# Optimization experiments

Measured on AMD Instinct MI355X. Metric: run time of the kernel, lower is better.

## Reference

```python
import jax, jax.numpy as jnp
import numpy as np

B, T, D_IN, D_SAE, K = 256, 8, 768, 8192, 32


def setup_inputs() -> dict:
    key = jax.random.key(0)
    k1, k2, k3 = jax.random.split(key, 3)
    x = jax.random.normal(k1, (B, T, D_IN), dtype=jnp.float32)
    # kaiming_uniform: bound = sqrt(6 / fan_in), fan_in = prod of trailing dims
    bound_e = float(np.sqrt(6.0 / (D_SAE * D_IN)))
    W_enc = jax.random.uniform(k2, (T, D_SAE, D_IN), jnp.float32, -bound_e, bound_e)
    bound_d = float(np.sqrt(6.0 / (D_IN * D_SAE)))
    W_dec = jax.random.uniform(k3, (T, D_IN, D_SAE), jnp.float32, -bound_d, bound_d)
    # decoder column normalization (norm over d_in axis), as in _normalize_decoder
    norms = jnp.clip(jnp.linalg.norm(W_dec, axis=1, keepdims=True), 1e-8)
    W_dec = W_dec / norms
    b_enc = jnp.zeros((T, D_SAE), jnp.float32)
    b_dec = jnp.zeros((T, D_IN), jnp.float32)
    return {"x": x, "W_enc": W_enc, "b_enc": b_enc, "W_dec": W_dec,
            "b_dec": b_dec, "k": K}


def reference(x, W_enc, b_enc, W_dec, b_dec, k):
    # x: (B, T, d_in)
    x_c = x - b_dec[None]                                   # (B, T, d)
    pre = jnp.einsum('btd,thd->bth', x_c, W_enc) + b_enc[None]  # (B, T, h)
    bt = pre.shape[0] * pre.shape[1]
    pre_flat = pre.reshape(bt, -1)
    topk_vals, topk_idx = jax.lax.top_k(pre_flat, k)        # (BT, k)
    rows = jnp.arange(bt)[:, None]
    u_flat = jnp.zeros_like(pre_flat).at[rows, topk_idx].set(jax.nn.relu(topk_vals))
    u = u_flat.reshape(pre.shape)                            # (B, T, h)
    x_hat = jnp.einsum('bth,tdh->btd', u, W_dec) + b_dec[None]
    recon_loss = jnp.mean(jnp.sum((x_hat - x) ** 2, axis=-1))
    return recon_loss, x_hat, u
```

## Files before the change

kernel.cpp:

```cpp
#include <hip/hip_runtime.h>
#include <cstdint>
#include <cstddef>

constexpr int B_SZ  = 256;
constexpr int T_SZ  = 8;
constexpr int DIN   = 768;
constexpr int DSAE  = 8192;
constexpr int KSEL  = 32;
constexpr int NROWS = B_SZ * T_SZ;
constexpr int CAND_CAP = 64;
constexpr int RCAP  = 32;
constexpr float EPS_W = 2e-4f;

constexpr size_t XC_SZ    = (size_t)NROWS * DIN;
constexpr size_t OFF_XC   = 0;
constexpr size_t OFF_SIDX = OFF_XC + XC_SZ;
constexpr size_t OFF_SVAL = OFF_SIDX + (size_t)NROWS * KSEL;
constexpr size_t OFF_WT   = OFF_SVAL + (size_t)NROWS * KSEL;
constexpr size_t WT_WORDS = (size_t)T_SZ * DSAE * DIN / 2;
constexpr size_t WS_FAST_WORDS = OFF_WT + WT_WORDS;

typedef short bf16x8 __attribute__((ext_vector_type(8)));
typedef float f32x4  __attribute__((ext_vector_type(4)));

__device__ inline unsigned rne1(float x) {
  unsigned u = __float_as_uint(x);
  return (u + 0x7FFFu + ((u >> 16) & 1u)) >> 16;
}
__device__ inline float fromb(unsigned h) { return __uint_as_float(h << 16); }
__device__ inline float bf16tof(unsigned short v) {
  return __uint_as_float((unsigned)v << 16);
}

__global__ void k_zero(float* p) { *p = 0.f; }

__global__ __launch_bounds__(256) void k_xc(const float* __restrict__ x,
                                            const float* __restrict__ bdec,
                                            float* __restrict__ xc) {
  int n = NROWS * DIN;
  for (int i = blockIdx.x * 256 + threadIdx.x; i < n; i += gridDim.x * 256) {
    int d = i % DIN;
    int t = (i / DIN) & (T_SZ - 1);
    xc[i] = x[i] - bdec[t * DIN + d];
  }
}

__global__ __launch_bounds__(512, 2) void k_encoder_split(const float* __restrict__ xc,
                                                          const float* __restrict__ Wenc,
                                                          const float* __restrict__ benc,
                                                          float* __restrict__ pre) {
  const int t  = blockIdx.y;
  const int n0 = blockIdx.x * 256;
  constexpr int NS = DIN / 32;
  constexpr int LO = 256 * 32;
  __shared__ __align__(16) short As[2][256 * 32];
  __shared__ __align__(16) short Bs[2][256 * 32 * 2];
  const int tid = threadIdx.x;

  const int srow = tid >> 1;
  const int kh   = (tid & 1) * 16;
  const float* aG = xc   + ((size_t)srow * T_SZ + t) * DIN + kh;
  const float* bG = Wenc + ((size_t)t * DSAE + n0 + srow) * DIN + kh;
  const int ssw = (srow & 3) ^ ((srow >> 2) & 3);
  const int c0 = (kh >> 3) + 0, c1 = (kh >> 3) + 1;
  const int wOff0 = srow * 32 + ((c0 ^ ssw) << 3);
  const int wOff1 = srow * 32 + ((c1 ^ ssw) << 3);

  auto loadG = [&](const float* base, int s, float4 (&R)[4]) {
    const float* p = base + s * 32;
    R[0] = *(const float4*)p;       R[1] = *(const float4*)(p + 4);
    R[2] = *(const float4*)(p + 8); R[3] = *(const float4*)(p + 12);
  };
  auto stageA = [&](float4 (&R)[4], int buf) {
    uint4 U;
    U.x = rne1(R[0].x) | (rne1(R[0].y) << 16); U.y = rne1(R[0].z) | (rne1(R[0].w) << 16);
    U.z = rne1(R[1].x) | (rne1(R[1].y) << 16); U.w = rne1(R[1].z) | (rne1(R[1].w) << 16);
    *(uint4*)&As[buf][wOff0] = U;
    U.x = rne1(R[2].x) | (rne1(R[2].y) << 16); U.y = rne1(R[2].z) | (rne1(R[2].w) << 16);
    U.z = rne1(R[3].x) | (rne1(R[3].y) << 16); U.w = rne1(R[3].z) | (rne1(R[3].w) << 16);
    *(uint4*)&As[buf][wOff1] = U;
  };
  auto stageB = [&](float4 (&R)[4], int buf) {
    float wv[16];
    *(float4*)&wv[0] = R[0]; *(float4*)&wv[4]  = R[1];
    *(float4*)&wv[8] = R[2]; *(float4*)&wv[12] = R[3];
    unsigned hh[16], ll[16];
#pragma unroll
    for (int i = 0; i < 16; ++i) {
      unsigned h = rne1(wv[i]);
      float res = wv[i] - fromb(h);
      hh[i] = h; ll[i] = rne1(res);
    }
    uint4 U;
    U.x = hh[0] | (hh[1] << 16);  U.y = hh[2] | (hh[3] << 16);
    U.z = hh[4] | (hh[5] << 16);  U.w = hh[6] | (hh[7] << 16);
    *(uint4*)&Bs[buf][wOff0] = U;
    U.x = hh[8] | (hh[9] << 16);  U.y = hh[10] | (hh[11] << 16);
    U.z = hh[12] | (hh[13] << 16); U.w = hh[14] | (hh[15] << 16);
    *(uint4*)&Bs[buf][wOff1] = U;
    U.x = ll[0] | (ll[1] << 16);  U.y = ll[2] | (ll[3] << 16);
    U.z = ll[4] | (ll[5] << 16);  U.w = ll[6] | (ll[7] << 16);
    *(uint4*)&Bs[buf][wOff0 + LO] = U;
    U.x = ll[8] | (ll[9] << 16);  U.y = ll[10] | (ll[11] << 16);
    U.z = ll[12] | (ll[13] << 16); U.w = ll[14] | (ll[15] << 16);
    *(uint4*)&Bs[buf][wOff1 + LO] = U;
  };

  const int wid = tid >> 6, lane = tid & 63;
  const int wm = wid >> 1;
  const int wn = wid & 1;
  const int l15 = lane & 15, kc = lane >> 4;
  int aOff[4], bOff[8];
#pragma unroll
  for (int i = 0; i < 4; ++i) {
    int ra = wm * 64 + i * 16 + l15;
    aOff[i] = ra * 32 + ((kc ^ ((ra & 3) ^ ((ra >> 2) & 3))) << 3);
  }
#pragma unroll
  for (int j = 0; j < 8; ++j) {
    int rb = wn * 128 + j * 16 + l15;
    bOff[j] = rb * 32 + ((kc ^ ((rb & 3) ^ ((rb >> 2) & 3))) << 3);
  }

  f32x4 acc[4][8] = {};
  auto compute = [&](int buf) {
    __syncthreads();
#pragma unroll
    for (int pass = 0; pass < 2; ++pass) {
      const int po = pass * LO;
#pragma unroll
      for (int nh = 0; nh < 2; ++nh) {
        bf16x8 bfr[4];
#pragma unroll
        for (int q = 0; q < 4; ++q)
          bfr[q] = *(const bf16x8*)&Bs[buf][bOff[nh * 4 + q] + po];
#pragma unroll
        for (int mi = 0; mi < 4; ++mi) {
          bf16x8 a = *(const bf16x8*)&As[buf][aOff[mi]];
#pragma unroll
          for (int q = 0; q < 4; ++q)
            acc[mi][nh * 4 + q] = __builtin_amdgcn_mfma_f32_16x16x32_bf16(
                a, bfr[q], acc[mi][nh * 4 + q], 0, 0, 0);
        }
      }
    }
  };

  float4 aR[4], bR0[4], bR1[4];
  loadG(bG, 0, bR0); loadG(aG, 0, aR);
  stageA(aR, 0); stageB(bR0, 0);
  loadG(bG, 1, bR0); loadG(aG, 1, aR);
  loadG(bG, 2, bR1);
  int cur = 0;
  auto iter = [&](int s, float4 (&bR)[4]) {
    compute(cur);
    if (s + 1 < NS) {
      stageA(aR, cur ^ 1);
      stageB(bR, cur ^ 1);
      if (s + 3 < NS) loadG(bG, s + 3, bR);
      if (s + 2 < NS) loadG(aG, s + 2, aR);
    }
    cur ^= 1;
  };
  for (int s = 0; s < NS; s += 2) { iter(s, bR0); iter(s + 1, bR1); }

#pragma unroll
  for (int ni = 0; ni < 8; ++ni) {
    const int col = n0 + wn * 128 + ni * 16 + l15;
    const float bias = benc[(size_t)t * DSAE + col];
#pragma unroll
    for (int mi = 0; mi < 4; ++mi) {
      const int rbase = wm * 64 + mi * 16 + kc * 4;
#pragma unroll
      for (int j = 0; j < 4; ++j)
        pre[((size_t)(rbase + j) * T_SZ + t) * DSAE + col] = acc[mi][ni][j] + bias;
    }
  }
}

__global__ __launch_bounds__(256) void k_select(const float* __restrict__ xc,
                                                const float* __restrict__ Wenc,
                                                const float* __restrict__ benc,
                                                float* u,
                                                int* __restrict__ sel_idx,
                                                float* __restrict__ sel_val) {
  const int r = blockIdx.x, t = r & (T_SZ - 1);
  __shared__ float sp[DSAE];
  __shared__ float redf[4], redf2[4];
  __shared__ int   redi[4];
  __shared__ float cv[CAND_CAP]; __shared__ int ci[CAND_CAP];
  __shared__ float sv[CAND_CAP]; __shared__ int si[CAND_CAP];
  __shared__ float rv[RCAP];     __shared__ int ri[RCAP];
  __shared__ double rd[RCAP];
  __shared__ double xd[DIN];
  __shared__ int   s_n, s_nR, s_A, s_nW;
  const int tid = threadIdx.x, lane = tid & 63, w = tid >> 6;
  float* urow = u + (size_t)r * DSAE;

  float s1 = 0.f, s2 = 0.f;
  for (int sgm = 0; sgm < DSAE / 256; ++sgm) {
    float v = urow[tid + sgm * 256];
    sp[tid + sgm * 256] = v;
    s1 += v; s2 = fmaf(v, v, s2);
  }
  for (int off = 32; off; off >>= 1) {
    s1 += __shfl_down(s1, off); s2 += __shfl_down(s2, off);
  }
  if (lane == 0) { redf[w] = s1; redf2[w] = s2; }
  __syncthreads();
  const float mean = (redf[0] + redf[1] + redf[2] + redf[3]) * (1.f / DSAE);
  const float var  = (redf2[0] + redf2[1] + redf2[2] + redf2[3]) * (1.f / DSAE) - mean * mean;
  const float sd   = sqrtf(fmaxf(var, 1e-20f));

  auto countGE = [&](float th) -> int {
    int c = 0;
#pragma unroll
    for (int sgm = 0; sgm < DSAE / 256; ++sgm)
      c += (sp[tid + sgm * 256] >= th) ? 1 : 0;
    for (int off = 32; off; off >>= 1) c += __shfl_down(c, off);
    __syncthreads();
    if (lane == 0) redi[w] = c;
    __syncthreads();
    return redi[0] + redi[1] + redi[2] + redi[3];
  };

  float tlo = mean + 2.0f * sd, thi = mean + 3.5f * sd;
  for (int it = 0; it < 8 && countGE(tlo) < KSEL; ++it) tlo -= sd;
  float th = mean + 2.52f * sd;
  int c = countGE(th);
  for (int it = 0; it < 24 && (c < KSEL || c > CAND_CAP); ++it) {
    if (c > CAND_CAP) tlo = th; else thi = th;
    th = 0.5f * (tlo + thi);
    c = countGE(th);
  }
  if (c < KSEL) { th = tlo; c = countGE(th); }

  if (tid == 0) s_n = 0;
  __syncthreads();
  for (int sgm = 0; sgm < DSAE / 256; ++sgm) {
    int i = tid + sgm * 256;
    float v = sp[i];
    if (v >= th) {
      int p = atomicAdd(&s_n, 1);
      if (p < CAND_CAP) { cv[p] = v; ci[p] = i; }
    }
  }
  __syncthreads();
  const int n = s_n < CAND_CAP ? s_n : CAND_CAP;

  if (tid < n) {
    float v = cv[tid]; int id = ci[tid];
    int rk = 0;
    for (int j = 0; j < n; ++j) {
      float vj = cv[j];
      rk += (vj > v || (vj == v && ci[j] < id)) ? 1 : 0;
    }
    sv[rk] = v; si[rk] = id;
  }
  __syncthreads();

  const float v32 = sv[KSEL - 1];
  const float wlo = v32 - EPS_W, whi = v32 + EPS_W;
  if (tid == 0) {
    int A = 0;
    while (A < KSEL - 1 && sv[A] > whi) ++A;
    s_A = A;
    int e = A;
    while (e < n && sv[e] >= wlo) ++e;
    s_nW = e - A;
  }
  __syncthreads();
  const int A  = s_A;
  const int nW = s_nW < RCAP ? s_nW : RCAP;
  if (tid < nW) { rv[tid] = sv[A + tid]; ri[tid] = si[A + tid]; }
  if (tid == 0) s_nR = nW;
  __syncthreads();
  if (th > wlo) {
    for (int sgm = 0; sgm < DSAE / 256; ++sgm) {
      int i = tid + sgm * 256;
      float v = sp[i];
      if (v >= wlo && v < th) {
        int p = atomicAdd(&s_nR, 1);
        if (p < RCAP) { rv[p] = v; ri[p] = i; }
      }
    }
  }
  __syncthreads();
  const int nR = s_nR < RCAP ? s_nR : RCAP;

  if (nR >= 2) {
    for (int i = tid; i < DIN; i += 256) xd[i] = (double)xc[(size_t)r * DIN + i];
    __syncthreads();
    for (int j = w; j < nR; j += 4) {
      const int h = ri[j];
      const float* wrow = Wenc + ((size_t)t * DSAE + h) * DIN;
      double s = 0.0;
#pragma unroll
      for (int ss = 0; ss < DIN / 64; ++ss)
        s += xd[lane + 64 * ss] * (double)wrow[lane + 64 * ss];
      for (int off = 32; off; off >>= 1) s += __shfl_down(s, off);
      if (lane == 0) rd[j] = s + (double)benc[(size_t)t * DSAE + h];
    }
  } else if (nR == 1) {
    if (tid == 0) rd[0] = (double)rv[0];
  }
  __syncthreads();

  for (int sgm = 0; sgm < DSAE / 256; ++sgm) urow[tid + sgm * 256] = 0.f;
  __syncthreads();

  if (tid < A) {
    float val = fmaxf(sv[tid], 0.f);
    urow[si[tid]] = val;
    sel_idx[(size_t)r * KSEL + tid] = si[tid];
    sel_val[(size_t)r * KSEL + tid] = val;
  }
  const int need = KSEL - A;
  if (tid < nR) {
    double v = rd[tid]; int id = ri[tid];
    int rk = 0;
    for (int j = 0; j < nR; ++j) {
      double vj = rd[j];
      rk += (vj > v || (vj == v && ri[j] < id)) ? 1 : 0;
    }
    if (rk < need) {
      float val = fmaxf((float)v, 0.f);
      urow[id] = val;
      sel_idx[(size_t)r * KSEL + A + rk] = id;
      sel_val[(size_t)r * KSEL + A + rk] = val;
    }
  }
}

__global__ __launch_bounds__(256) void k_transpose(const float* __restrict__ W,
                                                   unsigned short* __restrict__ Wt) {
  __shared__ float s[32][33];
  const int t  = blockIdx.z;
  const int h0 = blockIdx.x * 32;
  const int d0 = blockIdx.y * 32;
  const int c  = threadIdx.x & 31, rr = threadIdx.x >> 5;
#pragma unroll
  for (int q = 0; q < 4; ++q) {
    int d = d0 + rr + q * 8;
    s[rr + q * 8][c] = W[((size_t)t * DIN + d) * DSAE + h0 + c];
  }
  __syncthreads();
#pragma unroll
  for (int q = 0; q < 4; ++q) {
    int h = h0 + rr + q * 8;
    Wt[((size_t)t * DSAE + h) * DIN + d0 + c] = (unsigned short)rne1(s[c][rr + q * 8]);
  }
}

template <bool TRANSPOSED>
__global__ __launch_bounds__(256) void k_decoder(const void* __restrict__ Wd_,
                                                 const float* __restrict__ x,
                                                 const float* __restrict__ bdec,
                                                 const int* __restrict__ sel_idx,
                                                 const float* __restrict__ sel_val,
                                                 float* __restrict__ xhat,
                                                 float* __restrict__ loss) {
  const int r = blockIdx.x, t = r & (T_SZ - 1);
  __shared__ int   si[KSEL];
  __shared__ float sv[KSEL];
  __shared__ float rbuf[4];
  const int tid = threadIdx.x;
  if (tid < KSEL) {
    si[tid] = sel_idx[(size_t)r * KSEL + tid] & (DSAE - 1);
    sv[tid] = sel_val[(size_t)r * KSEL + tid];
  }
  __syncthreads();

  float acc[3];
#pragma unroll
  for (int i = 0; i < 3; ++i) acc[i] = bdec[(size_t)t * DIN + tid + 256 * i];
#pragma unroll 4
  for (int j = 0; j < KSEL; ++j) {
    const int h = si[j];
    const float v = sv[j];
    if (TRANSPOSED) {
      const unsigned short* wrow =
          (const unsigned short*)Wd_ + ((size_t)t * DSAE + h) * DIN;
#pragma unroll
      for (int i = 0; i < 3; ++i)
        acc[i] = fmaf(v, bf16tof(wrow[tid + 256 * i]), acc[i]);
    } else {
      const float* Wd = (const float*)Wd_;
#pragma unroll
      for (int i = 0; i < 3; ++i)
        acc[i] = fmaf(v, Wd[((size_t)t * DIN + tid + 256 * i) * DSAE + h], acc[i]);
    }
  }
  float sq = 0.f;
#pragma unroll
  for (int i = 0; i < 3; ++i) {
    const int d = tid + 256 * i;
    const float xv = x[(size_t)r * DIN + d];
    xhat[(size_t)r * DIN + d] = acc[i];
    const float e = acc[i] - xv;
    sq = fmaf(e, e, sq);
  }
  for (int off = 32; off; off >>= 1) sq += __shfl_down(sq, off);
  if ((tid & 63) == 0) rbuf[tid >> 6] = sq;
  __syncthreads();
  if (tid == 0)
    atomicAdd(loss, (rbuf[0] + rbuf[1] + rbuf[2] + rbuf[3]) * (1.0f / NROWS));
}

extern "C" void kernel_launch(void* const* d_in, const int* in_sizes, int n_in,
                              void* d_out, int out_size, void* d_ws, size_t ws_size,
                              hipStream_t stream) {
  const float* x    = (const float*)d_in[0];
  const float* Wenc = (const float*)d_in[1];
  const float* benc = (const float*)d_in[2];
  const float* Wdec = (const float*)d_in[3];
  const float* bdec = (const float*)d_in[4];

  float* out  = (float*)d_out;
  float* loss = out;
  float* xhat = out + 1;
  float* u    = out + 1 + (size_t)NROWS * DIN;

  float*          wsf  = (float*)d_ws;
  float*          xc   = wsf + OFF_XC;
  int*            sidx = (int*)(wsf + OFF_SIDX);
  float*          sval = wsf + OFF_SVAL;
  unsigned short* wt   = (unsigned short*)(wsf + OFF_WT);
  const bool fast = ws_size >= WS_FAST_WORDS * sizeof(float);

  k_zero<<<1, 1, 0, stream>>>(loss);
  k_xc<<<1536, 256, 0, stream>>>(x, bdec, xc);
  k_encoder_split<<<dim3(DSAE / 256, T_SZ), 512, 0, stream>>>(xc, Wenc, benc, u);
  k_select<<<NROWS, 256, 0, stream>>>(xc, Wenc, benc, u, sidx, sval);
  if (fast) {
    k_transpose<<<dim3(DSAE / 32, DIN / 32, T_SZ), 256, 0, stream>>>(Wdec, wt);
    k_decoder<true><<<NROWS, 256, 0, stream>>>(wt, x, bdec, sidx, sval, xhat, loss);
  } else {
    k_decoder<false><<<NROWS, 256, 0, stream>>>(Wdec, x, bdec, sidx, sval, xhat, loss);
  }
}
```

Before: 259.6 us.

## Drop split-bf16 weight residual pass and read pre-converted bf16 activations in encoder

The encoder no longer splits W_enc into hi and lo bf16 halves, so it does one MFMA pass instead of two. Activations are converted to bf16 once in k_xc and read straight from global memory into registers instead of being staged through shared memory. Tiles shrink from 256x256 to 256x64 per block with 256 threads to raise occupancy. This loses the extra weight precision, which the select stage must absorb when it rechecks candidates, and each block now rereads A from global memory.

```diff
diff --git a/kernel.cpp b/kernel.cpp
--- a/kernel.cpp
+++ b/kernel.cpp
@@ -14,7 +14,9 @@
 
 constexpr size_t XC_SZ    = (size_t)NROWS * DIN;
 constexpr size_t OFF_XC   = 0;
-constexpr size_t OFF_SIDX = OFF_XC + XC_SZ;
+constexpr size_t OFF_XCB  = OFF_XC + XC_SZ;
+constexpr size_t XCB_WORDS = XC_SZ / 2;
+constexpr size_t OFF_SIDX = OFF_XCB + XCB_WORDS;
 constexpr size_t OFF_SVAL = OFF_SIDX + (size_t)NROWS * KSEL;
 constexpr size_t OFF_WT   = OFF_SVAL + (size_t)NROWS * KSEL;
 constexpr size_t WT_WORDS = (size_t)T_SZ * DSAE * DIN / 2;
@@ -27,7 +29,6 @@
   unsigned u = __float_as_uint(x);
   return (u + 0x7FFFu + ((u >> 16) & 1u)) >> 16;
 }
-__device__ inline float fromb(unsigned h) { return __uint_as_float(h << 16); }
 __device__ inline float bf16tof(unsigned short v) {
   return __uint_as_float((unsigned)v << 16);
 }
@@ -36,137 +37,88 @@
 
 __global__ __launch_bounds__(256) void k_xc(const float* __restrict__ x,
                                             const float* __restrict__ bdec,
-                                            float* __restrict__ xc) {
+                                            float* __restrict__ xc,
+                                            unsigned short* __restrict__ xcb) {
   int n = NROWS * DIN;
   for (int i = blockIdx.x * 256 + threadIdx.x; i < n; i += gridDim.x * 256) {
     int d = i % DIN;
     int t = (i / DIN) & (T_SZ - 1);
-    xc[i] = x[i] - bdec[t * DIN + d];
-  }
-}
-
-__global__ __launch_bounds__(512, 2) void k_encoder_split(const float* __restrict__ xc,
-                                                          const float* __restrict__ Wenc,
-                                                          const float* __restrict__ benc,
-                                                          float* __restrict__ pre) {
+    float v = x[i] - bdec[t * DIN + d];
+    xc[i] = v;
+    xcb[i] = (unsigned short)rne1(v);
+  }
+}
+
+__global__ __launch_bounds__(256, 4) void k_encoder(const unsigned short* __restrict__ xcb,
+                                                    const float* __restrict__ Wenc,
+                                                    const float* __restrict__ benc,
+                                                    float* __restrict__ pre) {
   const int t  = blockIdx.y;
-  const int n0 = blockIdx.x * 256;
+  const int n0 = blockIdx.x * 64;
   constexpr int NS = DIN / 32;
-  constexpr int LO = 256 * 32;
-  __shared__ __align__(16) short As[2][256 * 32];
-  __shared__ __align__(16) short Bs[2][256 * 32 * 2];
+  __shared__ __align__(16) short Bs[2][64 * 32];
   const int tid = threadIdx.x;
 
-  const int srow = tid >> 1;
-  const int kh   = (tid & 1) * 16;
-  const float* aG = xc   + ((size_t)srow * T_SZ + t) * DIN + kh;
-  const float* bG = Wenc + ((size_t)t * DSAE + n0 + srow) * DIN + kh;
-  const int ssw = (srow & 3) ^ ((srow >> 2) & 3);
-  const int c0 = (kh >> 3) + 0, c1 = (kh >> 3) + 1;
-  const int wOff0 = srow * 32 + ((c0 ^ ssw) << 3);
-  const int wOff1 = srow * 32 + ((c1 ^ ssw) << 3);
-
-  auto loadG = [&](const float* base, int s, float4 (&R)[4]) {
-    const float* p = base + s * 32;
-    R[0] = *(const float4*)p;       R[1] = *(const float4*)(p + 4);
-    R[2] = *(const float4*)(p + 8); R[3] = *(const float4*)(p + 12);
+  const int srow = tid >> 2;
+  const int sq   = tid & 3;
+  const float* bG = Wenc + ((size_t)t * DSAE + n0 + srow) * DIN + sq * 8;
+  const int sssw = (srow & 3) ^ ((srow >> 2) & 3);
+  const int wOff = srow * 32 + ((sq ^ sssw) << 3);
+  float4 r0, r1;
+  auto loadB = [&](int s) {
+    const float* p = bG + s * 32;
+    r0 = *(const float4*)p; r1 = *(const float4*)(p + 4);
   };
-  auto stageA = [&](float4 (&R)[4], int buf) {
+  auto stage = [&](int buf) {
     uint4 U;
-    U.x = rne1(R[0].x) | (rne1(R[0].y) << 16); U.y = rne1(R[0].z) | (rne1(R[0].w) << 16);
-    U.z = rne1(R[1].x) | (rne1(R[1].y) << 16); U.w = rne1(R[1].z) | (rne1(R[1].w) << 16);
-    *(uint4*)&As[buf][wOff0] = U;
-    U.x = rne1(R[2].x) | (rne1(R[2].y) << 16); U.y = rne1(R[2].z) | (rne1(R[2].w) << 16);
-    U.z = rne1(R[3].x) | (rne1(R[3].y) << 16); U.w = rne1(R[3].z) | (rne1(R[3].w) << 16);
-    *(uint4*)&As[buf][wOff1] = U;
+    U.x = rne1(r0.x) | (rne1(r0.y) << 16); U.y = rne1(r0.z) | (rne1(r0.w) << 16);
+    U.z = rne1(r1.x) | (rne1(r1.y) << 16); U.w = rne1(r1.z) | (rne1(r1.w) << 16);
+    *(uint4*)&Bs[buf][wOff] = U;
   };
-  auto stageB = [&](float4 (&R)[4], int buf) {
-    float wv[16];
-    *(float4*)&wv[0] = R[0]; *(float4*)&wv[4]  = R[1];
-    *(float4*)&wv[8] = R[2]; *(float4*)&wv[12] = R[3];
-    unsigned hh[16], ll[16];
-#pragma unroll
-    for (int i = 0; i < 16; ++i) {
-      unsigned h = rne1(wv[i]);
-      float res = wv[i] - fromb(h);
-      hh[i] = h; ll[i] = rne1(res);
-    }
-    uint4 U;
-    U.x = hh[0] | (hh[1] << 16);  U.y = hh[2] | (hh[3] << 16);
-    U.z = hh[4] | (hh[5] << 16);  U.w = hh[6] | (hh[7] << 16);
-    *(uint4*)&Bs[buf][wOff0] = U;
-    U.x = hh[8] | (hh[9] << 16);  U.y = hh[10] | (hh[11] << 16);
-    U.z = hh[12] | (hh[13] << 16); U.w = hh[14] | (hh[15] << 16);
-    *(uint4*)&Bs[buf][wOff1] = U;
-    U.x = ll[0] | (ll[1] << 16);  U.y = ll[2] | (ll[3] << 16);
-    U.z = ll[4] | (ll[5] << 16);  U.w = ll[6] | (ll[7] << 16);
-    *(uint4*)&Bs[buf][wOff0 + LO] = U;
-    U.x = ll[8] | (ll[9] << 16);  U.y = ll[10] | (ll[11] << 16);
-    U.z = ll[12] | (ll[13] << 16); U.w = ll[14] | (ll[15] << 16);
-    *(uint4*)&Bs[buf][wOff1 + LO] = U;
-  };
-
-  const int wid = tid >> 6, lane = tid & 63;
-  const int wm = wid >> 1;
-  const int wn = wid & 1;
+
+  const int wm = tid >> 6, lane = tid & 63;
   const int l15 = lane & 15, kc = lane >> 4;
-  int aOff[4], bOff[8];
-#pragma unroll
-  for (int i = 0; i < 4; ++i) {
-    int ra = wm * 64 + i * 16 + l15;
-    aOff[i] = ra * 32 + ((kc ^ ((ra & 3) ^ ((ra >> 2) & 3))) << 3);
-  }
-#pragma unroll
-  for (int j = 0; j < 8; ++j) {
-    int rb = wn * 128 + j * 16 + l15;
-    bOff[j] = rb * 32 + ((kc ^ ((rb & 3) ^ ((rb >> 2) & 3))) << 3);
-  }
-
-  f32x4 acc[4][8] = {};
-  auto compute = [&](int buf) {
+  const unsigned short* aBase =
+      xcb + ((size_t)(wm * 64 + l15) * T_SZ + t) * DIN + kc * 8;
+  constexpr size_t A_MI = (size_t)16 * T_SZ * DIN;
+  int bOff[4];
+#pragma unroll
+  for (int ni = 0; ni < 4; ++ni) {
+    int row = ni * 16 + l15;
+    bOff[ni] = row * 32 + ((kc ^ ((row & 3) ^ ((row >> 2) & 3))) << 3);
+  }
+
+  f32x4 acc[4][4] = {};
+  bf16x8 a[4];
+  loadB(0); stage(0); loadB(1);
+#pragma unroll
+  for (int mi = 0; mi < 4; ++mi)
+    a[mi] = *(const bf16x8*)(aBase + mi * A_MI);
+  int cur = 0;
+  for (int s = 0; s < NS; ++s) {
     __syncthreads();
-#pragma unroll
-    for (int pass = 0; pass < 2; ++pass) {
-      const int po = pass * LO;
-#pragma unroll
-      for (int nh = 0; nh < 2; ++nh) {
-        bf16x8 bfr[4];
-#pragma unroll
-        for (int q = 0; q < 4; ++q)
-          bfr[q] = *(const bf16x8*)&Bs[buf][bOff[nh * 4 + q] + po];
-#pragma unroll
-        for (int mi = 0; mi < 4; ++mi) {
-          bf16x8 a = *(const bf16x8*)&As[buf][aOff[mi]];
-#pragma unroll
-          for (int q = 0; q < 4; ++q)
-            acc[mi][nh * 4 + q] = __builtin_amdgcn_mfma_f32_16x16x32_bf16(
-                a, bfr[q], acc[mi][nh * 4 + q], 0, 0, 0);
-        }
-      }
-    }
-  };
-
-  float4 aR[4], bR0[4], bR1[4];
-  loadG(bG, 0, bR0); loadG(aG, 0, aR);
-  stageA(aR, 0); stageB(bR0, 0);
-  loadG(bG, 1, bR0); loadG(aG, 1, aR);
-  loadG(bG, 2, bR1);
-  int cur = 0;
-  auto iter = [&](int s, float4 (&bR)[4]) {
-    compute(cur);
+    bf16x8 bf[4];
+#pragma unroll
+    for (int ni = 0; ni < 4; ++ni) bf[ni] = *(const bf16x8*)&Bs[cur][bOff[ni]];
+#pragma unroll
+    for (int mi = 0; mi < 4; ++mi)
+#pragma unroll
+      for (int ni = 0; ni < 4; ++ni)
+        acc[mi][ni] = __builtin_amdgcn_mfma_f32_16x16x32_bf16(
+            a[mi], bf[ni], acc[mi][ni], 0, 0, 0);
     if (s + 1 < NS) {
-      stageA(aR, cur ^ 1);
-      stageB(bR, cur ^ 1);
-      if (s + 3 < NS) loadG(bG, s + 3, bR);
-      if (s + 2 < NS) loadG(aG, s + 2, aR);
+      stage(cur ^ 1);
+#pragma unroll
+      for (int mi = 0; mi < 4; ++mi)
+        a[mi] = *(const bf16x8*)(aBase + (s + 1) * 32 + mi * A_MI);
+      if (s + 2 < NS) loadB(s + 2);
     }
     cur ^= 1;
-  };
-  for (int s = 0; s < NS; s += 2) { iter(s, bR0); iter(s + 1, bR1); }
-
-#pragma unroll
-  for (int ni = 0; ni < 8; ++ni) {
-    const int col = n0 + wn * 128 + ni * 16 + l15;
+  }
+
+#pragma unroll
+  for (int ni = 0; ni < 4; ++ni) {
+    const int col = n0 + ni * 16 + l15;
     const float bias = benc[(size_t)t * DSAE + col];
 #pragma unroll
     for (int mi = 0; mi < 4; ++mi) {
@@ -423,14 +375,15 @@
 
   float*          wsf  = (float*)d_ws;
   float*          xc   = wsf + OFF_XC;
+  unsigned short* xcb  = (unsigned short*)(wsf + OFF_XCB);
   int*            sidx = (int*)(wsf + OFF_SIDX);
   float*          sval = wsf + OFF_SVAL;
   unsigned short* wt   = (unsigned short*)(wsf + OFF_WT);
   const bool fast = ws_size >= WS_FAST_WORDS * sizeof(float);
 
   k_zero<<<1, 1, 0, stream>>>(loss);
-  k_xc<<<1536, 256, 0, stream>>>(x, bdec, xc);
-  k_encoder_split<<<dim3(DSAE / 256, T_SZ), 512, 0, stream>>>(xc, Wenc, benc, u);
+  k_xc<<<1536, 256, 0, stream>>>(x, bdec, xc, xcb);
+  k_encoder<<<dim3(DSAE / 64, T_SZ), 256, 0, stream>>>(xcb, Wenc, benc, u);
   k_select<<<NROWS, 256, 0, stream>>>(xc, Wenc, benc, u, sidx, sval);
   if (fast) {
     k_transpose<<<dim3(DSAE / 32, DIN / 32, T_SZ), 256, 0, stream>>>(Wdec, wt);
```

Measured after the change: 258.7 us. Within noise of the previous version (-0.4%).
